# Optimization experiments

Hardware: AMD Instinct MI355X
Metric: run time of the kernel (lower is better)

The kernel has to match this reference:

```python
import jax, jax.numpy as jnp
import numpy as np
from jax import lax

K = 20
SLOPE = 0.01


def setup_inputs() -> dict:
    key = jax.random.key(0)
    k1, k2 = jax.random.split(key)
    x = jax.random.normal(k1, (8, 64, 4096), dtype=jnp.float32)
    # Conv2d(2*64, 64, kernel_size=1, bias=False) weight, squeezed to (out, in)
    W = jax.random.normal(k2, (64, 128), dtype=jnp.float32) * 0.05
    return {"x": x, "W": W}


def reference(x, W):
    # x: (B, C, N), W: (O, 2C)
    B, C, N = x.shape
    # --- knn: pairwise_distance[b,i,j] = -||x_i||^2 + 2 x_i.x_j - ||x_j||^2 ---
    xx = jnp.sum(x * x, axis=1)                      # (B, N)
    inner = jnp.einsum('bcn,bcm->bnm', x, x)         # (B, N, N)
    pdist = 2.0 * inner - xx[:, :, None] - xx[:, None, :]
    idx = lax.top_k(pdist, K)[1]                     # (B, N, K) neighbor indices
    # --- get_graph_feature: gather neighbors, diff + center concat ---
    x_t = jnp.transpose(x, (0, 2, 1))                # (B, N, C)
    neigh = x_t[jnp.arange(B)[:, None, None], idx]   # (B, N, K, C)
    center = x_t[:, :, None, :]                      # (B, N, 1, C)
    feat = jnp.concatenate(
        [neigh - center, jnp.broadcast_to(center, (B, N, K, C))], axis=-1
    )                                                # (B, N, K, 2C)
    # --- 1x1 conv (no bias) + LeakyReLU ---
    h = jnp.einsum('bnkd,od->bonk', feat, W)         # (B, O, N, K)
    h = jnp.where(h >= 0, h, SLOPE * h)
    # --- max over neighbors ---
    return jnp.max(h, axis=-1)                       # (B, O, N)
```

## Files before the change

### kernel.cpp

```cpp
#include <hip/hip_runtime.h>
#include <cfloat>

#define B_ 8
#define C_ 64
#define N_ 4096
#define K_ 20
#define MARGIN 0.08f
#define CAP 64

typedef float f32x4v  __attribute__((ext_vector_type(4)));
typedef float f32x16v __attribute__((ext_vector_type(16)));
typedef _Float16 f16x8 __attribute__((ext_vector_type(8)));
typedef unsigned long long u64;

#define OFF_IDX 131072
#define OFF_QG  2752512
#define OFF_P0  19529728
#define OFF_P1  23724032

__device__ __forceinline__ void gll16(const void* g, void* l) {
    __builtin_amdgcn_global_load_lds(
        (const __attribute__((address_space(1))) unsigned int*)g,
        (__attribute__((address_space(3))) unsigned int*)l, 16, 0, 0);
}

__global__ __launch_bounds__(256) void k_split(const float* __restrict__ x,
                                               unsigned short* __restrict__ p0,
                                               unsigned short* __restrict__ p1,
                                               float* __restrict__ xxn) {
    __shared__ double sred[256];
    int b = blockIdx.x & 7, mt = blockIdx.x >> 3;
    int tid = threadIdx.x;
    int seg = tid >> 5, ml = tid & 31;
    int m = mt * 32 + ml;
    const float* xb = x + (size_t)b * C_ * N_;
    double ss = 0.0;
    unsigned short h0[8], h1[8];
#pragma unroll
    for (int j = 0; j < 8; ++j) {
        float v = xb[(size_t)(seg * 8 + j) * N_ + m];
        ss += (double)v * (double)v;
        _Float16 a = (_Float16)v;
        float r = v - (float)a;
        _Float16 bq = (_Float16)(r * 4096.f);
        h0[j] = __builtin_bit_cast(unsigned short, a);
        h1[j] = __builtin_bit_cast(unsigned short, bq);
    }
    uint4 q0, q1;
    q0.x = h0[0] | (h0[1] << 16); q0.y = h0[2] | (h0[3] << 16);
    q0.z = h0[4] | (h0[5] << 16); q0.w = h0[6] | (h0[7] << 16);
    q1.x = h1[0] | (h1[1] << 16); q1.y = h1[2] | (h1[3] << 16);
    q1.z = h1[4] | (h1[5] << 16); q1.w = h1[6] | (h1[7] << 16);
    size_t o16 = (size_t)(b * 8 + seg) * N_ + m;
    ((uint4*)p0)[o16] = q0;
    ((uint4*)p1)[o16] = q1;
    sred[tid] = ss;
    __syncthreads();
    if (tid < 32) {
        double t = 0.0;
#pragma unroll
        for (int s = 0; s < 8; ++s) t += sred[s * 32 + tid];
        xxn[b * N_ + mt * 32 + tid] = (float)(-0.5 * t);
    }
}

__device__ __forceinline__ void score4(const char* sm, const float* xxs,
                                       int mlb, int mf, int h,
                                       const f16x8 b0[4], float s[16]) {
    f32x16v acc;
#pragma unroll
    for (int g2i = 0; g2i < 4; ++g2i) {
        f32x4v xv = *(const f32x4v*)&xxs[mlb + 4 * h + 8 * g2i];
#pragma unroll
        for (int q = 0; q < 4; ++q) acc[g2i * 4 + q] = xv[q];
    }
    __builtin_amdgcn_s_setprio(1);
#pragma unroll
    for (int kc = 0; kc < 4; ++kc) {
        int seg = kc * 2 + h;
        f16x8 a0 = __builtin_bit_cast(f16x8,
            *(const f32x4v*)(sm + seg * 4096 + (mlb + mf) * 16));
        acc = __builtin_amdgcn_mfma_f32_32x32x16_f16(a0, b0[kc], acc, 0, 0, 0);
    }
    __builtin_amdgcn_s_setprio(0);
#pragma unroll
    for (int r = 0; r < 16; ++r) s[r] = acc[r];
}

__device__ __forceinline__ void score16(const char* sm, const float* xxs,
                                        int mlb, int mf, int h,
                                        const f16x8 b0[4], const f16x8 b1[4],
                                        float s[16]) {
    const float c12 = 1.f / 4096.f;
    f32x16v acc1, acc2;
#pragma unroll
    for (int g2i = 0; g2i < 4; ++g2i) {
        f32x4v xv = *(const f32x4v*)&xxs[mlb + 4 * h + 8 * g2i];
#pragma unroll
        for (int q = 0; q < 4; ++q) {
            acc1[g2i * 4 + q] = xv[q];
            acc2[g2i * 4 + q] = 0.f;
        }
    }
    __builtin_amdgcn_s_setprio(1);
#pragma unroll
    for (int kc = 0; kc < 4; ++kc) {
        int seg = kc * 2 + h;
        const char* pA = sm + seg * 4096 + (mlb + mf) * 16;
        f16x8 a0 = __builtin_bit_cast(f16x8, *(const f32x4v*)pA);
        f16x8 a1 = __builtin_bit_cast(f16x8, *(const f32x4v*)(pA + 32768));
        acc1 = __builtin_amdgcn_mfma_f32_32x32x16_f16(a0, b0[kc], acc1, 0, 0, 0);
        acc2 = __builtin_amdgcn_mfma_f32_32x32x16_f16(a0, b1[kc], acc2, 0, 0, 0);
        acc2 = __builtin_amdgcn_mfma_f32_32x32x16_f16(a1, b0[kc], acc2, 0, 0, 0);
    }
    __builtin_amdgcn_s_setprio(0);
#pragma unroll
    for (int r = 0; r < 16; ++r)
        s[r] = acc1[r] + acc2[r] * c12;
}

__global__ __launch_bounds__(512, 4) void k_topk(const unsigned short* __restrict__ p0g,
                                                 const unsigned short* __restrict__ p1g,
                                                 const float* __restrict__ xxn,
                                                 u64* bufg,
                                                 int* __restrict__ idxo,
                                                 const float* __restrict__ x,
                                                 const float* __restrict__ W,
                                                 float* qg) {
    __shared__ __align__(16) char smem[67328];
    int b = blockIdx.x & 7, nt = blockIdx.x >> 3;
    int n0 = nt * 64;
    int tid = threadIdx.x;
    int w = tid >> 6, l = tid & 63, h = l >> 5, mf = l & 31;
    int cs = w >> 1, wg = w & 1;
    int rowl = wg * 32 + mf;
    int b8 = b * 8;
    const f32x4v* g0 = (const f32x4v*)p0g;
    const f32x4v* g1 = (const f32x4v*)p1g;
    float* Mp   = (float*)(smem + 32768);
    float* xxs  = (float*)(smem + 65792);
    int*   cntp = (int*)(smem + 66816);
    float* T2p  = (float*)(smem + 67072);

    f16x8 b0[4], b1[4];
#pragma unroll
    for (int kc = 0; kc < 4; ++kc) {
        int seg = kc * 2 + h;
        size_t gi = (size_t)(b8 + seg) * N_ + n0 + rowl;
        b0[kc] = __builtin_bit_cast(f16x8, g0[gi]);
        b1[kc] = __builtin_bit_cast(f16x8, g1[gi]);
    }

#pragma unroll 1
    for (int ch = 0; ch < 16; ++ch) {
        __syncthreads();
#pragma unroll
        for (int i = 0; i < 4; ++i) {
            int lin = i * 512 + tid;
            int seg = lin >> 8, ml = lin & 255;
            gll16(g0 + ((size_t)(b8 + seg) * N_ + ch * 256 + ml),
                  smem + seg * 4096 + ml * 16);
        }
        if (tid < 256) xxs[tid] = xxn[b * N_ + ch * 256 + tid];
        __syncthreads();
#pragma unroll
        for (int t = 0; t < 2; ++t) {
            int mlb = cs * 64 + t * 32;
            float s[16];
            score4(smem, xxs, mlb, mf, h, b0, s);
            float m8[8];
#pragma unroll
            for (int r = 0; r < 8; ++r) m8[r] = fmaxf(s[r], s[r + 8]);
            float mx = fmaxf(fmaxf(fmaxf(m8[0], m8[1]), fmaxf(m8[2], m8[3])),
                             fmaxf(fmaxf(m8[4], m8[5]), fmaxf(m8[6], m8[7])));
            mx = fmaxf(mx, __shfl_xor(mx, 32));
            if (l < 32)
                Mp[rowl * 129 + ch * 8 + t * 4 + cs] = mx;
        }
    }

    __syncthreads();
    if (tid < 256) {
        int row = tid >> 2, q = tid & 3;
        const float* mrow = Mp + row * 129 + q * 32;
        float v8[8];
#pragma unroll
        for (int j = 0; j < 8; ++j) v8[j] = -FLT_MAX;
#pragma unroll
        for (int i = 0; i < 32; ++i) {
            float v = mrow[i];
#pragma unroll
            for (int j = 7; j >= 1; --j) {
                bool c1 = v > v8[j - 1];
                float nv = c1 ? v8[j - 1] : v;
                v8[j] = (v > v8[j]) ? nv : v8[j];
            }
            v8[0] = fmaxf(v8[0], v);
        }
        float* lp = (float*)smem + row * 33 + q * 8;
#pragma unroll
        for (int j = 0; j < 8; ++j) lp[j] = v8[j];
    }
    __syncthreads();
    if (tid < 64) {
        const float* lp = (const float*)smem + tid * 33;
        float hv0 = lp[0], hv1 = lp[8], hv2 = lp[16], hv3 = lp[24];
        int p0 = 0, p1 = 0, p2 = 0, p3 = 0;
        float tstar = -FLT_MAX;
        for (int k = 0; k < 20; ++k) {
            bool a = hv0 >= hv1; float ma = a ? hv0 : hv1; int sa = a ? 0 : 1;
            bool bb = hv2 >= hv3; float mb = bb ? hv2 : hv3; int sb = bb ? 2 : 3;
            bool c = ma >= mb; tstar = c ? ma : mb; int sl = c ? sa : sb;
            if (sl == 0) { ++p0; hv0 = (p0 < 8) ? lp[p0] : -FLT_MAX; }
            else if (sl == 1) { ++p1; hv1 = (p1 < 8) ? lp[8 + p1] : -FLT_MAX; }
            else if (sl == 2) { ++p2; hv2 = (p2 < 8) ? lp[16 + p2] : -FLT_MAX; }
            else { ++p3; hv3 = (p3 < 8) ? lp[24 + p3] : -FLT_MAX; }
        }
        T2p[tid] = tstar - MARGIN;
        cntp[tid] = 0;
    }
    __syncthreads();
    float T2r = T2p[rowl];

#pragma unroll 1
    for (int ch = 0; ch < 16; ++ch) {
        __syncthreads();
#pragma unroll
        for (int i = 0; i < 8; ++i) {
            int lin = i * 512 + tid;
            int panel = lin >> 11;
            int rem = lin & 2047;
            int seg = rem >> 8, ml = rem & 255;
            const f32x4v* src = panel ? g1 : g0;
            gll16(src + ((size_t)(b8 + seg) * N_ + ch * 256 + ml),
                  smem + panel * 32768 + seg * 4096 + ml * 16);
        }
        if (tid < 256) xxs[tid] = xxn[b * N_ + ch * 256 + tid];
        __syncthreads();
#pragma unroll
        for (int t = 0; t < 2; ++t) {
            int mlb = cs * 64 + t * 32;
            float s[16];
            score16(smem, xxs, mlb, mf, h, b0, b1, s);
            unsigned msk = 0;
#pragma unroll
            for (int r = 0; r < 16; ++r) msk |= (s[r] >= T2r) ? (1u << r) : 0u;
            int cb = ch * 256 + mlb + 4 * h;
            while (msk) {
                int r = __ffs(msk) - 1;
                msk &= msk - 1;
                int cand = cb + (r & 3) + 8 * (r >> 2);
                float sv = s[r];
                unsigned sb = __float_as_uint(sv);
                unsigned kk = (sv < 0.f) ? ~sb : (sb | 0x80000000u);
                int slot = atomicAdd(cntp + rowl, 1);
                if (slot < CAP)
                    bufg[((size_t)(b * N_ + n0 + rowl)) * CAP + slot] =
                        ((u64)kk << 32) | (unsigned)(~cand);
            }
        }
    }

    __syncthreads();
    u64*   keys = (u64*)(smem + 33536);
    float* Wl   = (float*)smem;
#pragma unroll
    for (int i = 0; i < 8; ++i) {
        int p = i * 512 + tid;
        int row = p >> 6, slot = p & 63;
        int c_ = cntp[row]; c_ = (c_ > CAP) ? CAP : c_;
        u64 key = 0;
        if (slot < c_)
            key = bufg[((size_t)(b * N_ + n0 + row)) * CAP + slot];
        keys[row * (CAP + 1) + slot] = key;
    }
#pragma unroll
    for (int i = 0; i < 16; ++i) {
        int lin = i * 512 + tid;
        int c = lin & 63, o2 = lin >> 6;
        float wv;
        if (o2 < 64) wv = W[o2 * 128 + c];
        else { int o = o2 - 64; wv = W[o * 128 + 64 + c] - W[o * 128 + c]; }
        Wl[c * 129 + o2] = wv;
    }
    __syncthreads();

    if (tid < 64) {
        int c_ = cntp[tid]; c_ = (c_ > CAP) ? CAP : c_;
        u64* kp = keys + tid * (CAP + 1);
        int* op = idxo + ((size_t)b * N_ + n0 + tid) * K_;
        for (int k = 0; k < K_; ++k) {
            u64 best = 0; int bs = 0;
            for (int s2 = 0; s2 < c_; ++s2) {
                bool g = kp[s2] > best;
                best = g ? kp[s2] : best;
                bs = g ? s2 : bs;
            }
            op[k] = (int)(~(unsigned)best) & 0xFFF;
            kp[bs] = 0;
        }
    }

    {
        int u = l, g8 = w;
        const float* xb = x + (size_t)b * C_ * N_ + n0 + g8 * 8;
        float a0[8], a1[8];
#pragma unroll
        for (int j = 0; j < 8; ++j) { a0[j] = 0.f; a1[j] = 0.f; }
#pragma unroll 4
        for (int c = 0; c < 64; ++c) {
            float2 wv = *(const float2*)&Wl[c * 129 + 2 * u];
            float4 v0 = *(const float4*)&xb[(size_t)c * N_];
            float4 v1 = *(const float4*)&xb[(size_t)c * N_ + 4];
            a0[0] += wv.x * v0.x; a1[0] += wv.y * v0.x;
            a0[1] += wv.x * v0.y; a1[1] += wv.y * v0.y;
            a0[2] += wv.x * v0.z; a1[2] += wv.y * v0.z;
            a0[3] += wv.x * v0.w; a1[3] += wv.y * v0.w;
            a0[4] += wv.x * v1.x; a1[4] += wv.y * v1.x;
            a0[5] += wv.x * v1.y; a1[5] += wv.y * v1.y;
            a0[6] += wv.x * v1.z; a1[6] += wv.y * v1.z;
            a0[7] += wv.x * v1.w; a1[7] += wv.y * v1.w;
        }
#pragma unroll
        for (int j = 0; j < 8; ++j) {
            float2 o; o.x = a0[j]; o.y = a1[j];
            *(float2*)&qg[((size_t)b * N_ + n0 + g8 * 8 + j) * 128 + 2 * u] = o;
        }
    }
}

__global__ __launch_bounds__(256) void k_out(const float* __restrict__ qg,
                                             const int* __restrict__ idxi,
                                             float* __restrict__ out) {
    __shared__ float T[16][66];
    int b = blockIdx.x & 7, nt = blockIdx.x >> 3;
    int n0 = nt * 16;
    int tid = threadIdx.x;
    int w = tid >> 6, o = tid & 63;
    const float* qgb = qg + (size_t)b * N_ * 128;
    for (int i = 0; i < 4; ++i) {
        int nl = w * 4 + i;
        int n = n0 + nl;
        float gv = qgb[(size_t)n * 128 + 64 + o];
        const int* ip = idxi + ((size_t)b * N_ + n) * K_;
        float mx = -FLT_MAX;
#pragma unroll 5
        for (int k = 0; k < K_; ++k) {
            int ik = ip[k];
            float hh = qgb[(size_t)ik * 128 + o] + gv;
            hh = (hh >= 0.f) ? hh : 0.01f * hh;
            mx = fmaxf(mx, hh);
        }
        T[nl][o] = mx;
    }
    __syncthreads();
    int ow = tid >> 2, q = tid & 3;
    {
        int nl = q * 4;
        float4 v;
        v.x = T[nl + 0][ow]; v.y = T[nl + 1][ow];
        v.z = T[nl + 2][ow]; v.w = T[nl + 3][ow];
        *(float4*)&out[((size_t)b * 64 + ow) * N_ + n0 + nl] = v;
    }
}

extern "C" void kernel_launch(void* const* d_in, const int* in_sizes, int n_in,
                              void* d_out, int out_size, void* d_ws, size_t ws_size,
                              hipStream_t stream) {
    const float* x = (const float*)d_in[0];
    const float* W = (const float*)d_in[1];
    float* out = (float*)d_out;

    float*          xxn  = (float*)d_ws;
    int*            idx  = (int*)((char*)d_ws + OFF_IDX);
    float*          qg   = (float*)((char*)d_ws + OFF_QG);
    u64*            bufg = (u64*)((char*)d_ws + OFF_QG);
    unsigned short* p0   = (unsigned short*)((char*)d_ws + OFF_P0);
    unsigned short* p1   = (unsigned short*)((char*)d_ws + OFF_P1);

    k_split<<<dim3(1024), dim3(256), 0, stream>>>(x, p0, p1, xxn);
    k_topk <<<dim3(512), dim3(512), 0, stream>>>(p0, p1, xxn, bufg, idx, x, W, qg);
    k_out  <<<dim3(2048), dim3(256), 0, stream>>>(qg, idx, out);
}
```

Baseline: 224.2 us.

## Load score-GEMM operands directly from global memory instead of LDS staging

Both scoring passes in the top-k kernel now read the A fragments and norm values straight from global memory into registers, replacing the cooperative global_load_lds staging into shared memory. This drops two block-wide barriers per chunk and lets waves run independently, with the chunk loop unrolled by two so loads can overlap MFMA work. In exchange, each wave fetches its own tile with no sharing through LDS, which duplicates global/L2 traffic across the warps that use the same columns and adds register pressure.

```diff
diff --git a/kernel.cpp b/kernel.cpp
--- a/kernel.cpp
+++ b/kernel.cpp
@@ -17,12 +17,6 @@
 #define OFF_QG  2752512
 #define OFF_P0  19529728
 #define OFF_P1  23724032
-
-__device__ __forceinline__ void gll16(const void* g, void* l) {
-    __builtin_amdgcn_global_load_lds(
-        (const __attribute__((address_space(1))) unsigned int*)g,
-        (__attribute__((address_space(3))) unsigned int*)l, 16, 0, 0);
-}
 
 __global__ __launch_bounds__(256) void k_split(const float* __restrict__ x,
                                                unsigned short* __restrict__ p0,
@@ -62,61 +56,6 @@
         for (int s = 0; s < 8; ++s) t += sred[s * 32 + tid];
         xxn[b * N_ + mt * 32 + tid] = (float)(-0.5 * t);
     }
-}
-
-__device__ __forceinline__ void score4(const char* sm, const float* xxs,
-                                       int mlb, int mf, int h,
-                                       const f16x8 b0[4], float s[16]) {
-    f32x16v acc;
-#pragma unroll
-    for (int g2i = 0; g2i < 4; ++g2i) {
-        f32x4v xv = *(const f32x4v*)&xxs[mlb + 4 * h + 8 * g2i];
-#pragma unroll
-        for (int q = 0; q < 4; ++q) acc[g2i * 4 + q] = xv[q];
-    }
-    __builtin_amdgcn_s_setprio(1);
-#pragma unroll
-    for (int kc = 0; kc < 4; ++kc) {
-        int seg = kc * 2 + h;
-        f16x8 a0 = __builtin_bit_cast(f16x8,
-            *(const f32x4v*)(sm + seg * 4096 + (mlb + mf) * 16));
-        acc = __builtin_amdgcn_mfma_f32_32x32x16_f16(a0, b0[kc], acc, 0, 0, 0);
-    }
-    __builtin_amdgcn_s_setprio(0);
-#pragma unroll
-    for (int r = 0; r < 16; ++r) s[r] = acc[r];
-}
-
-__device__ __forceinline__ void score16(const char* sm, const float* xxs,
-                                        int mlb, int mf, int h,
-                                        const f16x8 b0[4], const f16x8 b1[4],
-                                        float s[16]) {
-    const float c12 = 1.f / 4096.f;
-    f32x16v acc1, acc2;
-#pragma unroll
-    for (int g2i = 0; g2i < 4; ++g2i) {
-        f32x4v xv = *(const f32x4v*)&xxs[mlb + 4 * h + 8 * g2i];
-#pragma unroll
-        for (int q = 0; q < 4; ++q) {
-            acc1[g2i * 4 + q] = xv[q];
-            acc2[g2i * 4 + q] = 0.f;
-        }
-    }
-    __builtin_amdgcn_s_setprio(1);
-#pragma unroll
-    for (int kc = 0; kc < 4; ++kc) {
-        int seg = kc * 2 + h;
-        const char* pA = sm + seg * 4096 + (mlb + mf) * 16;
-        f16x8 a0 = __builtin_bit_cast(f16x8, *(const f32x4v*)pA);
-        f16x8 a1 = __builtin_bit_cast(f16x8, *(const f32x4v*)(pA + 32768));
-        acc1 = __builtin_amdgcn_mfma_f32_32x32x16_f16(a0, b0[kc], acc1, 0, 0, 0);
-        acc2 = __builtin_amdgcn_mfma_f32_32x32x16_f16(a0, b1[kc], acc2, 0, 0, 0);
-        acc2 = __builtin_amdgcn_mfma_f32_32x32x16_f16(a1, b0[kc], acc2, 0, 0, 0);
-    }
-    __builtin_amdgcn_s_setprio(0);
-#pragma unroll
-    for (int r = 0; r < 16; ++r)
-        s[r] = acc1[r] + acc2[r] * c12;
 }
 
 __global__ __launch_bounds__(512, 4) void k_topk(const unsigned short* __restrict__ p0g,
@@ -137,8 +76,8 @@
     int b8 = b * 8;
     const f32x4v* g0 = (const f32x4v*)p0g;
     const f32x4v* g1 = (const f32x4v*)p1g;
+    const float* xxb = xxn + (size_t)b * N_;
     float* Mp   = (float*)(smem + 32768);
-    float* xxs  = (float*)(smem + 65792);
     int*   cntp = (int*)(smem + 66816);
     float* T2p  = (float*)(smem + 67072);
 
@@ -151,26 +90,32 @@
         b1[kc] = __builtin_bit_cast(f16x8, g1[gi]);
     }
 
-#pragma unroll 1
+#pragma unroll 2
     for (int ch = 0; ch < 16; ++ch) {
-        __syncthreads();
-#pragma unroll
-        for (int i = 0; i < 4; ++i) {
-            int lin = i * 512 + tid;
-            int seg = lin >> 8, ml = lin & 255;
-            gll16(g0 + ((size_t)(b8 + seg) * N_ + ch * 256 + ml),
-                  smem + seg * 4096 + ml * 16);
-        }
-        if (tid < 256) xxs[tid] = xxn[b * N_ + ch * 256 + tid];
-        __syncthreads();
+        int cb = ch * 256;
 #pragma unroll
         for (int t = 0; t < 2; ++t) {
             int mlb = cs * 64 + t * 32;
-            float s[16];
-            score4(smem, xxs, mlb, mf, h, b0, s);
+            f32x16v acc;
+#pragma unroll
+            for (int g2i = 0; g2i < 4; ++g2i) {
+                f32x4v xv = *(const f32x4v*)&xxb[cb + mlb + 4 * h + 8 * g2i];
+#pragma unroll
+                for (int q = 0; q < 4; ++q) acc[g2i * 4 + q] = xv[q];
+            }
+            f16x8 a[4];
+#pragma unroll
+            for (int kc = 0; kc < 4; ++kc)
+                a[kc] = __builtin_bit_cast(f16x8,
+                    g0[(size_t)(b8 + kc * 2 + h) * N_ + cb + mlb + mf]);
+            __builtin_amdgcn_s_setprio(1);
+#pragma unroll
+            for (int kc = 0; kc < 4; ++kc)
+                acc = __builtin_amdgcn_mfma_f32_32x32x16_f16(a[kc], b0[kc], acc, 0, 0, 0);
+            __builtin_amdgcn_s_setprio(0);
             float m8[8];
 #pragma unroll
-            for (int r = 0; r < 8; ++r) m8[r] = fmaxf(s[r], s[r + 8]);
+            for (int r = 0; r < 8; ++r) m8[r] = fmaxf(acc[r], acc[r + 8]);
             float mx = fmaxf(fmaxf(fmaxf(m8[0], m8[1]), fmaxf(m8[2], m8[3])),
                              fmaxf(fmaxf(m8[4], m8[5]), fmaxf(m8[6], m8[7])));
             mx = fmaxf(mx, __shfl_xor(mx, 32));
@@ -222,34 +167,49 @@
     __syncthreads();
     float T2r = T2p[rowl];
 
-#pragma unroll 1
+    const float c12 = 1.f / 4096.f;
+#pragma unroll 2
     for (int ch = 0; ch < 16; ++ch) {
-        __syncthreads();
-#pragma unroll
-        for (int i = 0; i < 8; ++i) {
-            int lin = i * 512 + tid;
-            int panel = lin >> 11;
-            int rem = lin & 2047;
-            int seg = rem >> 8, ml = rem & 255;
-            const f32x4v* src = panel ? g1 : g0;
-            gll16(src + ((size_t)(b8 + seg) * N_ + ch * 256 + ml),
-                  smem + panel * 32768 + seg * 4096 + ml * 16);
-        }
-        if (tid < 256) xxs[tid] = xxn[b * N_ + ch * 256 + tid];
-        __syncthreads();
+        int cb = ch * 256;
 #pragma unroll
         for (int t = 0; t < 2; ++t) {
             int mlb = cs * 64 + t * 32;
+            f32x16v acc1, acc2;
+#pragma unroll
+            for (int g2i = 0; g2i < 4; ++g2i) {
+                f32x4v xv = *(const f32x4v*)&xxb[cb + mlb + 4 * h + 8 * g2i];
+#pragma unroll
+                for (int q = 0; q < 4; ++q) {
+                    acc1[g2i * 4 + q] = xv[q];
+                    acc2[g2i * 4 + q] = 0.f;
+                }
+            }
+            f16x8 a0[4], a1[4];
+#pragma unroll
+            for (int kc = 0; kc < 4; ++kc) {
+                size_t gi = (size_t)(b8 + kc * 2 + h) * N_ + cb + mlb + mf;
+                a0[kc] = __builtin_bit_cast(f16x8, g0[gi]);
+                a1[kc] = __builtin_bit_cast(f16x8, g1[gi]);
+            }
+            __builtin_amdgcn_s_setprio(1);
+#pragma unroll
+            for (int kc = 0; kc < 4; ++kc) {
+                acc1 = __builtin_amdgcn_mfma_f32_32x32x16_f16(a0[kc], b0[kc], acc1, 0, 0, 0);
+                acc2 = __builtin_amdgcn_mfma_f32_32x32x16_f16(a0[kc], b1[kc], acc2, 0, 0, 0);
+                acc2 = __builtin_amdgcn_mfma_f32_32x32x16_f16(a1[kc], b0[kc], acc2, 0, 0, 0);
+            }
+            __builtin_amdgcn_s_setprio(0);
             float s[16];
-            score16(smem, xxs, mlb, mf, h, b0, b1, s);
+#pragma unroll
+            for (int r = 0; r < 16; ++r) s[r] = acc1[r] + acc2[r] * c12;
             unsigned msk = 0;
 #pragma unroll
             for (int r = 0; r < 16; ++r) msk |= (s[r] >= T2r) ? (1u << r) : 0u;
-            int cb = ch * 256 + mlb + 4 * h;
+            int cbb = cb + mlb + 4 * h;
             while (msk) {
                 int r = __ffs(msk) - 1;
                 msk &= msk - 1;
-                int cand = cb + (r & 3) + 8 * (r >> 2);
+                int cand = cbb + (r & 3) + 8 * (r >> 2);
                 float sv = s[r];
                 unsigned sb = __float_as_uint(sv);
                 unsigned kk = (sv < 0.f) ? ~sb : (sb | 0x80000000u);
```

After: 247.5 us. +10.4%, slower.
